# Kernel optimization log

Measured on AMD Instinct MI355X. Metric: run time of the kernel, lower is better.

## Reference

```python
import jax, jax.numpy as jnp
import numpy as np

B, N, IN_DIM, OUT_DIM, MID_DIM, K = 4, 8192, 3, 64, 32, 16
EPS = 1e-5  # BatchNorm eps


def _bn_relu(x, gamma, beta):
    # x: [B, N, C]; BatchNorm1d in training mode -> batch stats over (B, N)
    mean = jnp.mean(x, axis=(0, 1))
    var = jnp.var(x, axis=(0, 1))
    return jax.nn.relu(gamma * (x - mean) * jax.lax.rsqrt(var + EPS) + beta)


def _gather(pts, idx):
    # pts: [B, N, C]; idx: [B, ...] int -> [B, ..., C]
    return jax.vmap(lambda p, i: p[i])(pts, idx)


def _fps(xyz, npoint):
    # farthest point sampling; xyz: [B, N, 3] -> idx [B, npoint]
    b, n, _ = xyz.shape

    def step(carry, _):
        dist, farthest = carry
        centroid = jnp.take_along_axis(xyz, farthest[:, None, None], axis=1)  # [B,1,3]
        d = jnp.sum((xyz - centroid) ** 2, axis=-1)  # [B,N]
        dist = jnp.minimum(dist, d)
        nxt = jnp.argmax(dist, axis=-1).astype(jnp.int32)
        return (dist, nxt), farthest

    init = (jnp.full((b, n), 1e10, xyz.dtype), jnp.zeros((b,), jnp.int32))
    _, idx = jax.lax.scan(step, init, None, length=npoint)
    return idx.T  # [B, npoint]


def _knn(query, ref, k):
    # query: [B,S,3], ref: [B,N,3] -> k nearest indices [B,S,k]
    d = (jnp.sum(query ** 2, -1, keepdims=True)
         - 2.0 * jnp.einsum('bsd,bnd->bsn', query, ref)
         + jnp.sum(ref ** 2, -1)[:, None, :])
    _, idx = jax.lax.top_k(-d, k)
    return idx


def setup_inputs() -> dict:
    key = jax.random.key(0)
    ks = jax.random.split(key, 13)
    sc = lambda fan_in: 1.0 / np.sqrt(fan_in)
    inp = {
        'x_in': jax.random.normal(ks[0], (B, N, IN_DIM), jnp.float32),
        # first_mlp: Conv1d(3,32,1) -> BN -> ReLU -> Conv1d(32,64,1)
        'W1': jax.random.uniform(ks[1], (MID_DIM, IN_DIM), jnp.float32, -sc(IN_DIM), sc(IN_DIM)),
        'b1': jax.random.uniform(ks[2], (MID_DIM,), jnp.float32, -sc(IN_DIM), sc(IN_DIM)),
        'g1': jnp.ones((MID_DIM,), jnp.float32),
        'be1': jnp.zeros((MID_DIM,), jnp.float32),
        'W2': jax.random.uniform(ks[3], (OUT_DIM, MID_DIM), jnp.float32, -sc(MID_DIM), sc(MID_DIM)),
        'b2': jax.random.uniform(ks[4], (OUT_DIM,), jnp.float32, -sc(MID_DIM), sc(MID_DIM)),
        # last_mlp: Conv1d(67,64,1) -> BN -> ReLU -> Conv1d(64,64,1)
        'W3': jax.random.uniform(ks[5], (OUT_DIM, OUT_DIM + IN_DIM), jnp.float32, -sc(OUT_DIM + IN_DIM), sc(OUT_DIM + IN_DIM)),
        'b3': jax.random.uniform(ks[6], (OUT_DIM,), jnp.float32, -sc(OUT_DIM + IN_DIM), sc(OUT_DIM + IN_DIM)),
        'g2': jnp.ones((OUT_DIM,), jnp.float32),
        'be2': jnp.zeros((OUT_DIM,), jnp.float32),
        'W4': jax.random.uniform(ks[7], (OUT_DIM, OUT_DIM), jnp.float32, -sc(OUT_DIM), sc(OUT_DIM)),
        'b4': jax.random.uniform(ks[8], (OUT_DIM,), jnp.float32, -sc(OUT_DIM), sc(OUT_DIM)),
    }
    return inp


def reference(x_in, W1, b1, g1, be1, W2, b2, W3, b3, g2, be2, W4, b4):
    # first_mlp (1x1 convs == per-point matmuls), [B,N,3] -> [B,N,64]
    h = _bn_relu(x_in @ W1.T + b1, g1, be1)
    feat = h @ W2.T + b2  # [B,N,64]

    # sample_and_group: FPS to N//2 centers, kNN grouping (indices are non-diff)
    xyz_c = jax.lax.stop_gradient(x_in)
    npoint = N // 2
    fidx = _fps(xyz_c, npoint)                      # [B,S]
    new_xyz = _gather(x_in, fidx)                   # [B,S,3]
    idx = _knn(_gather(xyz_c, fidx), xyz_c, K)      # [B,S,K]

    grouped_xyz = _gather(x_in, idx) - new_xyz[:, :, None, :]  # [B,S,K,3]
    grouped_feat = _gather(feat, idx)                          # [B,S,K,64]
    x_cat = jnp.concatenate([grouped_xyz, grouped_feat], axis=-1)  # [B,S,K,67]

    x = jnp.max(x_cat, axis=2)  # max over neighbors -> [B,S,67]

    # last_mlp, [B,S,67] -> [B,S,64]
    x = _bn_relu(x @ W3.T + b3, g2, be2)
    return x @ W4.T + b4
```

## Files before the change

### kernel.cpp

```cpp
#include <hip/hip_runtime.h>
#include <float.h>
#include <math.h>

#define NB 4
#define NPTS 8192
#define NS 4096
#define MIDC 32
#define OUTC 64
#define CATC 67
#define BN_EPS 1e-5f
#define TOTAL_PTS (NB*NPTS)
#define TOTAL_S (NB*NS)
#define KT2 1024
#define N_FEATX_ITEMS 128
#define N_KNN_ITEMS 256
#define N_WORKERS 128

__device__ __forceinline__ double packkey(double d, int sp) {
    return __longlong_as_double((__double_as_longlong(d) & 0xFFFFFFFFFFFFE000ULL)
                                | (unsigned long long)sp);
}

template<int CTRL, int RM>
__device__ __forceinline__ double dpp_fmax64(double v) {
    int lo = __builtin_amdgcn_update_dpp(0, __double2loint(v), CTRL, RM, 0xF, false);
    int hi = __builtin_amdgcn_update_dpp(0, __double2hiint(v), CTRL, RM, 0xF, false);
    return fmax(v, __hiloint2double(hi, lo));
}

__device__ __forceinline__ unsigned int mpart(unsigned int x) {
    x &= 1023u;
    x = (x | (x << 16)) & 0x030000FFu;
    x = (x | (x << 8))  & 0x0300F00Fu;
    x = (x | (x << 4))  & 0x030C30C3u;
    x = (x | (x << 2))  & 0x09249249u;
    return x;
}

__global__ void k_init(float* __restrict__ stats, double* __restrict__ mom, int* __restrict__ ctrs) {
    int tid = threadIdx.x;
    if (tid < 128) stats[64 + tid] = 0.f;
    if (tid < 9) mom[tid] = 0.0;
    if (tid < 2) ctrs[tid] = 0;
}

__global__ void __launch_bounds__(256) k_mom(const float* __restrict__ xin, double* __restrict__ mom) {
    int t = blockIdx.x * 256 + threadIdx.x;
    double sx = 0, sy = 0, sz = 0, sxx = 0, sxy = 0, sxz = 0, syy = 0, syz = 0, szz = 0;
#pragma unroll
    for (int j = 0; j < 4; j++) {
        int p = t * 4 + j;
        double x = (double)xin[p * 3], y = (double)xin[p * 3 + 1], z = (double)xin[p * 3 + 2];
        sx += x; sy += y; sz += z;
        sxx = fma(x, x, sxx); sxy = fma(x, y, sxy); sxz = fma(x, z, sxz);
        syy = fma(y, y, syy); syz = fma(y, z, syz); szz = fma(z, z, szz);
    }
#pragma unroll
    for (int off = 32; off; off >>= 1) {
        sx += __shfl_down(sx, off); sy += __shfl_down(sy, off); sz += __shfl_down(sz, off);
        sxx += __shfl_down(sxx, off); sxy += __shfl_down(sxy, off); sxz += __shfl_down(sxz, off);
        syy += __shfl_down(syy, off); syz += __shfl_down(syz, off); szz += __shfl_down(szz, off);
    }
    if ((threadIdx.x & 63) == 0) {
        atomicAdd(&mom[0], sx); atomicAdd(&mom[1], sy); atomicAdd(&mom[2], sz);
        atomicAdd(&mom[3], sxx); atomicAdd(&mom[4], sxy); atomicAdd(&mom[5], sxz);
        atomicAdd(&mom[6], syy); atomicAdd(&mom[7], syz); atomicAdd(&mom[8], szz);
    }
}

__global__ void k_bn1stats(const double* __restrict__ mom, const float* __restrict__ W1,
                           const float* __restrict__ b1, float* __restrict__ stats) {
    int c = threadIdx.x;
    double n = (double)TOTAL_PTS;
    double mx = mom[0] / n, my = mom[1] / n, mz = mom[2] / n;
    double Cxx = mom[3] / n - mx * mx, Cxy = mom[4] / n - mx * my, Cxz = mom[5] / n - mx * mz;
    double Cyy = mom[6] / n - my * my, Cyz = mom[7] / n - my * mz, Czz = mom[8] / n - mz * mz;
    double wx = (double)W1[c * 3], wy = (double)W1[c * 3 + 1], wz = (double)W1[c * 3 + 2];
    double mu = wx * mx + wy * my + wz * mz + (double)b1[c];
    double var = wx * wx * Cxx + wy * wy * Cyy + wz * wz * Czz
               + 2.0 * (wx * wy * Cxy + wx * wz * Cxz + wy * wz * Cyz);
    stats[c] = (float)mu;
    stats[32 + c] = rsqrtf(fmaxf((float)var, 0.f) + BN_EPS);
}

union MU {
    struct { float4 spts[NPTS]; double swd[2][16]; float bbx[16][6]; } f;
    struct { float sxf[KT2], syf[KT2], szf[KT2]; double mk[4][16][64]; } k;
    struct { float W2s[OUTC * MIDC]; float w1s[MIDC * 3], b1s[MIDC], p1[MIDC], p2[MIDC]; } x;
    struct { float W3s[OUTC * CATC]; float x67[4][68]; float lsum[64], lsq[64]; } g;
};

__device__ void do_fps(MU& u, const float* __restrict__ xin, int* __restrict__ fidx) {
    const int b = blockIdx.x;
    const int tid = threadIdx.x;
    const int lane = tid & 63, w = tid >> 6;
    const float* xb = xin + (size_t)b * NPTS * 3;

    float mnx = FLT_MAX, mny = FLT_MAX, mnz = FLT_MAX;
    float mxx = -FLT_MAX, mxy = -FLT_MAX, mxz = -FLT_MAX;
    for (int j = 0; j < 8; j++) {
        int p = tid + (j << 10);
        float x = xb[p * 3], y = xb[p * 3 + 1], z = xb[p * 3 + 2];
        mnx = fminf(mnx, x); mny = fminf(mny, y); mnz = fminf(mnz, z);
        mxx = fmaxf(mxx, x); mxy = fmaxf(mxy, y); mxz = fmaxf(mxz, z);
    }
#pragma unroll
    for (int off = 32; off; off >>= 1) {
        mnx = fminf(mnx, __shfl_xor(mnx, off)); mny = fminf(mny, __shfl_xor(mny, off));
        mnz = fminf(mnz, __shfl_xor(mnz, off));
        mxx = fmaxf(mxx, __shfl_xor(mxx, off)); mxy = fmaxf(mxy, __shfl_xor(mxy, off));
        mxz = fmaxf(mxz, __shfl_xor(mxz, off));
    }
    if (lane == 0) {
        u.f.bbx[w][0] = mnx; u.f.bbx[w][1] = mny; u.f.bbx[w][2] = mnz;
        u.f.bbx[w][3] = mxx; u.f.bbx[w][4] = mxy; u.f.bbx[w][5] = mxz;
    }
    __syncthreads();
#pragma unroll
    for (int i = 0; i < 16; i++) {
        mnx = fminf(mnx, u.f.bbx[i][0]); mny = fminf(mny, u.f.bbx[i][1]);
        mnz = fminf(mnz, u.f.bbx[i][2]);
        mxx = fmaxf(mxx, u.f.bbx[i][3]); mxy = fmaxf(mxy, u.f.bbx[i][4]);
        mxz = fmaxf(mxz, u.f.bbx[i][5]);
    }
    float scx = 1023.0f / fmaxf(mxx - mnx, 1e-20f);
    float scy = 1023.0f / fmaxf(mxy - mny, 1e-20f);
    float scz = 1023.0f / fmaxf(mxz - mnz, 1e-20f);
    __syncthreads();

    unsigned long long* karr = (unsigned long long*)&u;
    for (int j = 0; j < 8; j++) {
        int p = tid + (j << 10);
        float x = xb[p * 3], y = xb[p * 3 + 1], z = xb[p * 3 + 2];
        unsigned int ix = (unsigned int)min(1023, max(0, (int)((x - mnx) * scx)));
        unsigned int iy = (unsigned int)min(1023, max(0, (int)((y - mny) * scy)));
        unsigned int iz = (unsigned int)min(1023, max(0, (int)((z - mnz) * scz)));
        unsigned long long code = (unsigned long long)((mpart(ix) << 2) | (mpart(iy) << 1) | mpart(iz));
        karr[p] = (code << 13) | (unsigned long long)p;
    }
    __syncthreads();
    for (int k = 2; k <= NPTS; k <<= 1) {
        for (int jj = k >> 1; jj > 0; jj >>= 1) {
            for (int pos = tid; pos < NPTS; pos += 1024) {
                int l2 = pos ^ jj;
                if (l2 > pos) {
                    unsigned long long a = karr[pos], c = karr[l2];
                    bool up = ((pos & k) == 0);
                    if ((up && a > c) || (!up && a < c)) { karr[pos] = c; karr[l2] = a; }
                }
            }
            __syncthreads();
        }
    }

    unsigned long long kk[8];
#pragma unroll
    for (int j = 0; j < 8; j++) kk[j] = karr[tid * 8 + j];
    __syncthreads();
    float blox = FLT_MAX, bloy = FLT_MAX, bloz = FLT_MAX;
    float bhix = -FLT_MAX, bhiy = -FLT_MAX, bhiz = -FLT_MAX;
    double dk[8];
#pragma unroll
    for (int j = 0; j < 8; j++) {
        int oi = (int)(kk[j] & 0x1FFFULL);
        float x = xb[oi * 3], y = xb[oi * 3 + 1], z = xb[oi * 3 + 2];
        int sp = tid * 8 + j;
        int slot = (sp >> 3) | ((sp & 7) << 10);
        u.f.spts[slot] = make_float4(x, y, z, __int_as_float(oi));
        blox = fminf(blox, x); bloy = fminf(bloy, y); bloz = fminf(bloz, z);
        bhix = fmaxf(bhix, x); bhiy = fmaxf(bhiy, y); bhiz = fmaxf(bhiz, z);
        dk[j] = packkey(1e10, sp);
    }
    if (tid == 0)
        __hip_atomic_store(&fidx[b * NS], 0, __ATOMIC_RELAXED, __HIP_MEMORY_SCOPE_AGENT);
    __syncthreads();

    float cxf = xb[0], cyf = xb[1], czf = xb[2];
    double cx = (double)cxf, cy = (double)cyf, cz = (double)czf;
    double tmax = packkey(1e10, tid * 8 + 7);
    double wm = 0.0;
    for (int t = 1; t < NS; t++) {
        float exf = fmaxf(fmaxf(blox - cxf, cxf - bhix), 0.f);
        float eyf = fmaxf(fmaxf(bloy - cyf, cyf - bhiy), 0.f);
        float ezf = fmaxf(fmaxf(bloz - czf, czf - bhiz), 0.f);
        float dmsqf = fmaf(exf, exf, fmaf(eyf, eyf, ezf * ezf));
        double tupper = __longlong_as_double(__double_as_longlong(tmax) | 0x1FFFULL);
        bool doupd = !((double)dmsqf * 0.99999 > tupper);
        if (__any(doupd)) {
            if (doupd) {
                double t0 = 0.0, t1 = 0.0;
#pragma unroll
                for (int j = 0; j < 8; j += 2) {
                    float4 v0 = u.f.spts[tid | (j << 10)];
                    float4 v1 = u.f.spts[tid | ((j + 1) << 10)];
                    double dx0 = (double)v0.x - cx, dy0 = (double)v0.y - cy, dz0 = (double)v0.z - cz;
                    double d0 = fma(dx0, dx0, fma(dy0, dy0, dz0 * dz0));
                    double nk0 = fmin(dk[j], packkey(d0, tid * 8 + j));
                    dk[j] = nk0; t0 = fmax(t0, nk0);
                    double dx1 = (double)v1.x - cx, dy1 = (double)v1.y - cy, dz1 = (double)v1.z - cz;
                    double d1 = fma(dx1, dx1, fma(dy1, dy1, dz1 * dz1));
                    double nk1 = fmin(dk[j + 1], packkey(d1, tid * 8 + j + 1));
                    dk[j + 1] = nk1; t1 = fmax(t1, nk1);
                }
                tmax = fmax(t0, t1);
            }
            double v = tmax;
            v = dpp_fmax64<0x121, 0xF>(v);
            v = dpp_fmax64<0x122, 0xF>(v);
            v = dpp_fmax64<0x124, 0xF>(v);
            v = dpp_fmax64<0x128, 0xF>(v);
            v = dpp_fmax64<0x142, 0xa>(v);
            v = dpp_fmax64<0x143, 0x8>(v);
            int wlo = __builtin_amdgcn_readlane(__double2loint(v), 63);
            int whi = __builtin_amdgcn_readlane(__double2hiint(v), 63);
            wm = __hiloint2double(whi, wlo);
        }
        if (lane == 0) u.f.swd[t & 1][w] = wm;
        __syncthreads();
        double gv = u.f.swd[t & 1][lane & 15];
        gv = dpp_fmax64<0x121, 0xF>(gv);
        gv = dpp_fmax64<0x122, 0xF>(gv);
        gv = dpp_fmax64<0x124, 0xF>(gv);
        gv = dpp_fmax64<0x128, 0xF>(gv);
        int sp = (int)((unsigned int)__double_as_longlong(gv) & 0x1FFFu);
        float4 cw = u.f.spts[(sp >> 3) | ((sp & 7) << 10)];
        cxf = cw.x; cyf = cw.y; czf = cw.z;
        cx = (double)cxf; cy = (double)cyf; cz = (double)czf;
        if (tid == 0)
            __hip_atomic_store(&fidx[b * NS + t], __float_as_int(cw.w),
                               __ATOMIC_RELAXED, __HIP_MEMORY_SCOPE_AGENT);
    }
}

__device__ void do_featx(MU& u, int item, const float* __restrict__ xin, const float* __restrict__ stats,
                         const float* __restrict__ W1, const float* __restrict__ b1,
                         const float* __restrict__ g1, const float* __restrict__ be1,
                         const float* __restrict__ W2, const float* __restrict__ b2,
                         float* __restrict__ feat, int* __restrict__ ctrs) {
    int tid = threadIdx.x;
    for (int i = tid; i < OUTC * MIDC; i += 256) u.x.W2s[i] = W2[i];
    if (tid < MIDC * 3) u.x.w1s[tid] = W1[tid];
    if (tid < MIDC) {
        u.x.b1s[tid] = b1[tid];
        u.x.p1[tid] = stats[32 + tid] * g1[tid];
        u.x.p2[tid] = be1[tid] - stats[tid] * stats[32 + tid] * g1[tid];
    }
    __syncthreads();
    int p = item * 256 + tid;
    float x = xin[p * 3], y = xin[p * 3 + 1], z = xin[p * 3 + 2];
    float h[MIDC];
#pragma unroll
    for (int c = 0; c < MIDC; c++) {
        float v = fmaf(u.x.w1s[c * 3 + 2], z, fmaf(u.x.w1s[c * 3 + 1], y, fmaf(u.x.w1s[c * 3], x, u.x.b1s[c])));
        h[c] = fmaxf(fmaf(v, u.x.p1[c], u.x.p2[c]), 0.f);
    }
#pragma unroll 4
    for (int o = 0; o < OUTC; o++) {
        float a = b2[o];
#pragma unroll
        for (int c = 0; c < MIDC; c++) a = fmaf(u.x.W2s[o * MIDC + c], h[c], a);
        feat[p * OUTC + o] = a;
    }
    __syncthreads();
    if (tid == 0)
        __hip_atomic_fetch_add(&ctrs[1], 1, __ATOMIC_RELEASE, __HIP_MEMORY_SCOPE_AGENT);
}

__device__ void do_knn_group(MU& u, int* qarr, int item, const float* __restrict__ xin,
                             const int* __restrict__ fidx, int* __restrict__ knn,
                             const float* __restrict__ feat,
                             const float* __restrict__ W3, const float* __restrict__ b3,
                             float* __restrict__ y3, float* __restrict__ stats,
                             int* __restrict__ ctrs) {
    int tid = threadIdx.x;
    int part = tid >> 6;
    int ql = tid & 63;
    int b = (item * 64) >> 12;
    const float* xb = xin + (size_t)b * NPTS * 3;
    if (tid < 64) {
        unsigned int qv;
        for (;;) {
            qv = (unsigned int)__hip_atomic_load(&fidx[item * 64 + tid],
                                                 __ATOMIC_RELAXED, __HIP_MEMORY_SCOPE_AGENT);
            if (qv <= 8191u) break;
            __builtin_amdgcn_s_sleep(64);
        }
        qarr[tid] = (int)qv;
    }
    __syncthreads();
    int qi = qarr[ql];
    float qxf = xb[qi * 3], qyf = xb[qi * 3 + 1], qzf = xb[qi * 3 + 2];
    double qx = (double)qxf, qy = (double)qyf, qz = (double)qzf;
    double kd0 = DBL_MAX, kd1 = DBL_MAX, kd2 = DBL_MAX, kd3 = DBL_MAX,
           kd4 = DBL_MAX, kd5 = DBL_MAX, kd6 = DBL_MAX, kd7 = DBL_MAX,
           kd8 = DBL_MAX, kd9 = DBL_MAX, kd10 = DBL_MAX, kd11 = DBL_MAX,
           kd12 = DBL_MAX, kd13 = DBL_MAX, kd14 = DBL_MAX, kd15 = DBL_MAX;
    float kd15f = FLT_MAX;
    for (int tile = 0; tile < NPTS / KT2; tile++) {
        for (int m = tid; m < KT2; m += 256) {
            int gj = tile * KT2 + m;
            u.k.sxf[m] = xb[gj * 3]; u.k.syf[m] = xb[gj * 3 + 1]; u.k.szf[m] = xb[gj * 3 + 2];
        }
        __syncthreads();
        int base = part * (KT2 / 4);
        for (int m = 0; m < KT2 / 4; m++) {
            int li = base + m;
            float fdx = qxf - u.k.sxf[li], fdy = qyf - u.k.syf[li], fdz = qzf - u.k.szf[li];
            float d32 = fmaf(fdx, fdx, fmaf(fdy, fdy, fdz * fdz));
            if (d32 <= kd15f) {
                double dx = qx - (double)u.k.sxf[li], dy = qy - (double)u.k.syf[li], dz = qz - (double)u.k.szf[li];
                double d = fma(dx, dx, fma(dy, dy, dz * dz));
                double key = __longlong_as_double(
                    (__double_as_longlong(d) & 0xFFFFFFFFFFFFE000ULL)
                    | (unsigned long long)(tile * KT2 + li));
                if (key < kd15) {
                    kd15 = fmax(kd14, fmin(kd15, key)); kd14 = fmax(kd13, fmin(kd14, key));
                    kd13 = fmax(kd12, fmin(kd13, key)); kd12 = fmax(kd11, fmin(kd12, key));
                    kd11 = fmax(kd10, fmin(kd11, key)); kd10 = fmax(kd9,  fmin(kd10, key));
                    kd9  = fmax(kd8,  fmin(kd9,  key)); kd8  = fmax(kd7,  fmin(kd8,  key));
                    kd7  = fmax(kd6,  fmin(kd7,  key)); kd6  = fmax(kd5,  fmin(kd6,  key));
                    kd5  = fmax(kd4,  fmin(kd5,  key)); kd4  = fmax(kd3,  fmin(kd4,  key));
                    kd3  = fmax(kd2,  fmin(kd3,  key)); kd2  = fmax(kd1,  fmin(kd2,  key));
                    kd1  = fmax(kd0,  fmin(kd1,  key)); kd0  = fmin(kd0,  key);
                    kd15f = (kd15 >= DBL_MAX) ? FLT_MAX
                          : __double2float_ru(kd15) * (1.0f + 1e-5f);
                }
            }
        }
        __syncthreads();
    }
    u.k.mk[part][0][ql] = kd0;  u.k.mk[part][1][ql] = kd1;  u.k.mk[part][2][ql] = kd2;  u.k.mk[part][3][ql] = kd3;
    u.k.mk[part][4][ql] = kd4;  u.k.mk[part][5][ql] = kd5;  u.k.mk[part][6][ql] = kd6;  u.k.mk[part][7][ql] = kd7;
    u.k.mk[part][8][ql] = kd8;  u.k.mk[part][9][ql] = kd9;  u.k.mk[part][10][ql] = kd10; u.k.mk[part][11][ql] = kd11;
    u.k.mk[part][12][ql] = kd12; u.k.mk[part][13][ql] = kd13; u.k.mk[part][14][ql] = kd14; u.k.mk[part][15][ql] = kd15;
    __syncthreads();
    if (tid < 64) {
        int i0 = 0, i1 = 0, i2 = 0, i3 = 0;
        double h0 = u.k.mk[0][0][tid], h1 = u.k.mk[1][0][tid], h2 = u.k.mk[2][0][tid], h3 = u.k.mk[3][0][tid];
        int* outp = knn + (size_t)(item * 64 + tid) * 16;
#pragma unroll
        for (int k = 0; k < 16; k++) {
            double mm = fmin(fmin(h0, h1), fmin(h2, h3));
            outp[k] = (int)(__double_as_longlong(mm) & 0x1FFFULL);
            if (mm == h0)      { i0++; h0 = (i0 < 16) ? u.k.mk[0][i0][tid] : DBL_MAX; }
            else if (mm == h1) { i1++; h1 = (i1 < 16) ? u.k.mk[1][i1][tid] : DBL_MAX; }
            else if (mm == h2) { i2++; h2 = (i2 < 16) ? u.k.mk[2][i2][tid] : DBL_MAX; }
            else               { i3++; h3 = (i3 < 16) ? u.k.mk[3][i3][tid] : DBL_MAX; }
        }
    }
    if (tid == 0) {
        while (__hip_atomic_load(&ctrs[1], __ATOMIC_ACQUIRE, __HIP_MEMORY_SCOPE_AGENT) < N_FEATX_ITEMS)
            __builtin_amdgcn_s_sleep(64);
    }
    __syncthreads();

    int w = tid >> 6, lane = tid & 63;
    for (int i = tid; i < OUTC * CATC; i += 256) u.g.W3s[i] = W3[i];
    if (tid < 64) { u.g.lsum[tid] = 0.f; u.g.lsq[tid] = 0.f; }
    __syncthreads();
    float bb3 = b3[lane];
    float psum = 0.f, psq = 0.f;
    int p0 = item * 64 + w * 16;
    for (int it = 0; it < 16; it++) {
        int p = p0 + it;
        int pb = p >> 12;
        int myidx = knn[p * 16 + (lane & 15)];
        int nbk[16];
#pragma unroll
        for (int k = 0; k < 16; k++) nbk[k] = __shfl(myidx, k);
        float m = -FLT_MAX;
#pragma unroll
        for (int k = 0; k < 16; k++) m = fmaxf(m, feat[(size_t)(pb * NPTS + nbk[k]) * OUTC + lane]);
        u.g.x67[w][3 + lane] = m;
        if (lane < 3) {
            int ci = qarr[w * 16 + it];
            float cc = xin[(size_t)(pb * NPTS + ci) * 3 + lane];
            float mg = -FLT_MAX;
#pragma unroll
            for (int k = 0; k < 16; k++) mg = fmaxf(mg, xin[(size_t)(pb * NPTS + nbk[k]) * 3 + lane] - cc);
            u.g.x67[w][lane] = mg;
        }
        float acc = bb3;
#pragma unroll
        for (int c = 0; c < CATC; c++) acc = fmaf(u.g.W3s[lane * CATC + c], u.g.x67[w][c], acc);
        y3[(size_t)p * OUTC + lane] = acc;
        psum += acc; psq = fmaf(acc, acc, psq);
    }
    atomicAdd(&u.g.lsum[lane], psum);
    atomicAdd(&u.g.lsq[lane], psq);
    __syncthreads();
    if (tid < 64) { atomicAdd(&stats[64 + tid], u.g.lsum[tid]); atomicAdd(&stats[128 + tid], u.g.lsq[tid]); }
}

__global__ void __launch_bounds__(1024) k_mega(const float* __restrict__ xin,
                                               const float* __restrict__ W1, const float* __restrict__ b1,
                                               const float* __restrict__ g1, const float* __restrict__ be1,
                                               const float* __restrict__ W2, const float* __restrict__ b2,
                                               const float* __restrict__ W3, const float* __restrict__ b3,
                                               float* __restrict__ stats, float* __restrict__ feat,
                                               int* __restrict__ fidx, int* __restrict__ knn,
                                               float* __restrict__ y3, int* __restrict__ ctrs) {
    __shared__ MU u;
    __shared__ int s_item;
    __shared__ int qarr[64];
    if (blockIdx.x < NB) { do_fps(u, xin, fidx); return; }
    if (threadIdx.x >= 256) return;
    int tid = threadIdx.x;
    for (;;) {
        __syncthreads();
        if (tid == 0) s_item = atomicAdd(&ctrs[0], 1);
        __syncthreads();
        int item = s_item;
        if (item >= N_FEATX_ITEMS + N_KNN_ITEMS) return;
        if (item < N_FEATX_ITEMS)
            do_featx(u, item, xin, stats, W1, b1, g1, be1, W2, b2, feat, ctrs);
        else
            do_knn_group(u, qarr, item - N_FEATX_ITEMS, xin, fidx, knn, feat, W3, b3, y3, stats, ctrs);
    }
}

__global__ void k_stats2(float* __restrict__ stats) {
    int c = threadIdx.x;
    float m = stats[64 + c] / (float)TOTAL_S;
    float var = stats[128 + c] / (float)TOTAL_S - m * m;
    stats[192 + c] = m;
    stats[256 + c] = rsqrtf(var + BN_EPS);
}

__global__ void __launch_bounds__(256) k_last(const float* __restrict__ y3, const float* __restrict__ stats,
                                              const float* __restrict__ g2, const float* __restrict__ be2,
                                              const float* __restrict__ W4, const float* __restrict__ b4,
                                              float* __restrict__ out) {
    __shared__ float W4t[OUTC * OUTC];
    __shared__ float xs[4][64];
    int tid = threadIdx.x;
    for (int i = tid; i < OUTC * OUTC; i += 256) W4t[(i & 63) * 64 + (i >> 6)] = W4[i];
    int lp = tid >> 6, o = tid & 63;
    int p = blockIdx.x * 4 + lp;
    float v = y3[(size_t)p * OUTC + o];
    v = fmaf((v - stats[192 + o]) * stats[256 + o], g2[o], be2[o]);
    xs[lp][o] = fmaxf(v, 0.f);
    __syncthreads();
    const float* xp = xs[lp];
    float acc = b4[o];
#pragma unroll
    for (int c = 0; c < OUTC; c++) acc = fmaf(W4t[c * 64 + o], xp[c], acc);
    out[(size_t)p * OUTC + o] = acc;
}

extern "C" void kernel_launch(void* const* d_in, const int* in_sizes, int n_in,
                              void* d_out, int out_size, void* d_ws, size_t ws_size,
                              hipStream_t stream) {
    const float* xin = (const float*)d_in[0];
    const float* W1  = (const float*)d_in[1];
    const float* b1  = (const float*)d_in[2];
    const float* g1  = (const float*)d_in[3];
    const float* be1 = (const float*)d_in[4];
    const float* W2  = (const float*)d_in[5];
    const float* b2  = (const float*)d_in[6];
    const float* W3  = (const float*)d_in[7];
    const float* b3  = (const float*)d_in[8];
    const float* g2  = (const float*)d_in[9];
    const float* be2 = (const float*)d_in[10];
    const float* W4  = (const float*)d_in[11];
    const float* b4  = (const float*)d_in[12];
    float* out = (float*)d_out;

    float* ws = (float*)d_ws;
    float* feat = ws;
    int*   fidx = (int*)(feat + (size_t)TOTAL_PTS * OUTC);
    int*   knn  = fidx + TOTAL_S;
    float* y3   = (float*)(knn + (size_t)TOTAL_S * 16);
    float* stats = y3 + (size_t)TOTAL_S * OUTC;
    double* mom = (double*)(stats + 320);
    int* ctrs = (int*)(mom + 9);

    k_init<<<1, 256, 0, stream>>>(stats, mom, ctrs);
    k_mom<<<32, 256, 0, stream>>>(xin, mom);
    k_bn1stats<<<1, 32, 0, stream>>>(mom, W1, b1, stats);
    k_mega<<<NB + N_WORKERS, 1024, 0, stream>>>(xin, W1, b1, g1, be1, W2, b2, W3, b3,
                                                stats, feat, fidx, knn, y3, ctrs);
    k_stats2<<<1, 64, 0, stream>>>(stats);
    k_last<<<TOTAL_S / 4, 256, 0, stream>>>(y3, stats, g2, be2, W4, b4, out);
}
```

Baseline: 4.283 ms.

## Fold moment, BN stats, and final MLP stages into persistent mega-kernel work queue

Moves the moment reduction, BN1 stats, BN2 stats and final MLP into the persistent k_mega work queue as ordered item ranges, gated by global atomic counters with acquire/release spin-waits. This removes four separate kernel launches and the gaps between them. Worker block count is cut from 128 to 32, which reduces parallelism for the featx/knn/last items that run alongside FPS. Spin-waiting blocks may sit idle while dependencies finish.

```diff
diff --git a/kernel.cpp b/kernel.cpp
--- a/kernel.cpp
+++ b/kernel.cpp
@@ -12,9 +12,17 @@
 #define TOTAL_PTS (NB*NPTS)
 #define TOTAL_S (NB*NS)
 #define KT2 1024
+#define N_WORKERS 32
+
+#define IT_MOM0   0
+#define IT_BN1    32
+#define IT_FEATX0 33
+#define IT_KNN0   161
+#define IT_STATS2 417
+#define IT_LAST0  418
+#define IT_END    674
 #define N_FEATX_ITEMS 128
 #define N_KNN_ITEMS 256
-#define N_WORKERS 128
 
 __device__ __forceinline__ double packkey(double d, int sp) {
     return __longlong_as_double((__double_as_longlong(d) & 0xFFFFFFFFFFFFE000ULL)
@@ -41,46 +49,7 @@
     int tid = threadIdx.x;
     if (tid < 128) stats[64 + tid] = 0.f;
     if (tid < 9) mom[tid] = 0.0;
-    if (tid < 2) ctrs[tid] = 0;
-}
-
-__global__ void __launch_bounds__(256) k_mom(const float* __restrict__ xin, double* __restrict__ mom) {
-    int t = blockIdx.x * 256 + threadIdx.x;
-    double sx = 0, sy = 0, sz = 0, sxx = 0, sxy = 0, sxz = 0, syy = 0, syz = 0, szz = 0;
-#pragma unroll
-    for (int j = 0; j < 4; j++) {
-        int p = t * 4 + j;
-        double x = (double)xin[p * 3], y = (double)xin[p * 3 + 1], z = (double)xin[p * 3 + 2];
-        sx += x; sy += y; sz += z;
-        sxx = fma(x, x, sxx); sxy = fma(x, y, sxy); sxz = fma(x, z, sxz);
-        syy = fma(y, y, syy); syz = fma(y, z, syz); szz = fma(z, z, szz);
-    }
-#pragma unroll
-    for (int off = 32; off; off >>= 1) {
-        sx += __shfl_down(sx, off); sy += __shfl_down(sy, off); sz += __shfl_down(sz, off);
-        sxx += __shfl_down(sxx, off); sxy += __shfl_down(sxy, off); sxz += __shfl_down(sxz, off);
-        syy += __shfl_down(syy, off); syz += __shfl_down(syz, off); szz += __shfl_down(szz, off);
-    }
-    if ((threadIdx.x & 63) == 0) {
-        atomicAdd(&mom[0], sx); atomicAdd(&mom[1], sy); atomicAdd(&mom[2], sz);
-        atomicAdd(&mom[3], sxx); atomicAdd(&mom[4], sxy); atomicAdd(&mom[5], sxz);
-        atomicAdd(&mom[6], syy); atomicAdd(&mom[7], syz); atomicAdd(&mom[8], szz);
-    }
-}
-
-__global__ void k_bn1stats(const double* __restrict__ mom, const float* __restrict__ W1,
-                           const float* __restrict__ b1, float* __restrict__ stats) {
-    int c = threadIdx.x;
-    double n = (double)TOTAL_PTS;
-    double mx = mom[0] / n, my = mom[1] / n, mz = mom[2] / n;
-    double Cxx = mom[3] / n - mx * mx, Cxy = mom[4] / n - mx * my, Cxz = mom[5] / n - mx * mz;
-    double Cyy = mom[6] / n - my * my, Cyz = mom[7] / n - my * mz, Czz = mom[8] / n - mz * mz;
-    double wx = (double)W1[c * 3], wy = (double)W1[c * 3 + 1], wz = (double)W1[c * 3 + 2];
-    double mu = wx * mx + wy * my + wz * mz + (double)b1[c];
-    double var = wx * wx * Cxx + wy * wy * Cyy + wz * wz * Czz
-               + 2.0 * (wx * wy * Cxy + wx * wz * Cxz + wy * wz * Cyz);
-    stats[c] = (float)mu;
-    stats[32 + c] = rsqrtf(fmaxf((float)var, 0.f) + BN_EPS);
+    if (tid < 6) ctrs[tid] = 0;
 }
 
 union MU {
@@ -88,6 +57,7 @@
     struct { float sxf[KT2], syf[KT2], szf[KT2]; double mk[4][16][64]; } k;
     struct { float W2s[OUTC * MIDC]; float w1s[MIDC * 3], b1s[MIDC], p1[MIDC], p2[MIDC]; } x;
     struct { float W3s[OUTC * CATC]; float x67[4][68]; float lsum[64], lsq[64]; } g;
+    struct { float W4t[OUTC * OUTC]; float xs[4][64]; } l;
 };
 
 __device__ void do_fps(MU& u, const float* __restrict__ xin, int* __restrict__ fidx) {
@@ -232,12 +202,73 @@
     }
 }
 
+__device__ void do_mom(int item, const float* __restrict__ xin, double* __restrict__ mom,
+                       int* __restrict__ ctrs) {
+    int tid = threadIdx.x;
+    int t = item * 256 + tid;
+    double sx = 0, sy = 0, sz = 0, sxx = 0, sxy = 0, sxz = 0, syy = 0, syz = 0, szz = 0;
+#pragma unroll
+    for (int j = 0; j < 4; j++) {
+        int p = t * 4 + j;
+        double x = (double)xin[p * 3], y = (double)xin[p * 3 + 1], z = (double)xin[p * 3 + 2];
+        sx += x; sy += y; sz += z;
+        sxx = fma(x, x, sxx); sxy = fma(x, y, sxy); sxz = fma(x, z, sxz);
+        syy = fma(y, y, syy); syz = fma(y, z, syz); szz = fma(z, z, szz);
+    }
+#pragma unroll
+    for (int off = 32; off; off >>= 1) {
+        sx += __shfl_down(sx, off); sy += __shfl_down(sy, off); sz += __shfl_down(sz, off);
+        sxx += __shfl_down(sxx, off); sxy += __shfl_down(sxy, off); sxz += __shfl_down(sxz, off);
+        syy += __shfl_down(syy, off); syz += __shfl_down(syz, off); szz += __shfl_down(szz, off);
+    }
+    if ((tid & 63) == 0) {
+        atomicAdd(&mom[0], sx); atomicAdd(&mom[1], sy); atomicAdd(&mom[2], sz);
+        atomicAdd(&mom[3], sxx); atomicAdd(&mom[4], sxy); atomicAdd(&mom[5], sxz);
+        atomicAdd(&mom[6], syy); atomicAdd(&mom[7], syz); atomicAdd(&mom[8], szz);
+    }
+    __syncthreads();
+    if (tid == 0)
+        __hip_atomic_fetch_add(&ctrs[4], 1, __ATOMIC_RELEASE, __HIP_MEMORY_SCOPE_AGENT);
+}
+
+__device__ void do_bn1(const double* __restrict__ mom, const float* __restrict__ W1,
+                       const float* __restrict__ b1, float* __restrict__ stats,
+                       int* __restrict__ ctrs) {
+    int tid = threadIdx.x;
+    if (tid == 0) {
+        while (__hip_atomic_load(&ctrs[4], __ATOMIC_ACQUIRE, __HIP_MEMORY_SCOPE_AGENT) < 32)
+            __builtin_amdgcn_s_sleep(32);
+    }
+    __syncthreads();
+    if (tid < MIDC) {
+        int c = tid;
+        double n = (double)TOTAL_PTS;
+        double mx = mom[0] / n, my = mom[1] / n, mz = mom[2] / n;
+        double Cxx = mom[3] / n - mx * mx, Cxy = mom[4] / n - mx * my, Cxz = mom[5] / n - mx * mz;
+        double Cyy = mom[6] / n - my * my, Cyz = mom[7] / n - my * mz, Czz = mom[8] / n - mz * mz;
+        double wx = (double)W1[c * 3], wy = (double)W1[c * 3 + 1], wz = (double)W1[c * 3 + 2];
+        double mu = wx * mx + wy * my + wz * mz + (double)b1[c];
+        double var = wx * wx * Cxx + wy * wy * Cyy + wz * wz * Czz
+                   + 2.0 * (wx * wy * Cxy + wx * wz * Cxz + wy * wz * Cyz);
+        stats[c] = (float)mu;
+        stats[32 + c] = rsqrtf(fmaxf((float)var, 0.f) + BN_EPS);
+    }
+    __syncthreads();
+    if (tid == 0)
+        __hip_atomic_store(&ctrs[5], 1, __ATOMIC_RELEASE, __HIP_MEMORY_SCOPE_AGENT);
+}
+
 __device__ void do_featx(MU& u, int item, const float* __restrict__ xin, const float* __restrict__ stats,
                          const float* __restrict__ W1, const float* __restrict__ b1,
                          const float* __restrict__ g1, const float* __restrict__ be1,
                          const float* __restrict__ W2, const float* __restrict__ b2,
                          float* __restrict__ feat, int* __restrict__ ctrs) {
     int tid = threadIdx.x;
+    if (tid == 0) {
+        while (__hip_atomic_load(&ctrs[5], __ATOMIC_ACQUIRE, __HIP_MEMORY_SCOPE_AGENT) < 1)
+            __builtin_amdgcn_s_sleep(32);
+    }
+    __syncthreads();
     for (int i = tid; i < OUTC * MIDC; i += 256) u.x.W2s[i] = W2[i];
     if (tid < MIDC * 3) u.x.w1s[tid] = W1[tid];
     if (tid < MIDC) {
@@ -390,6 +421,55 @@
     atomicAdd(&u.g.lsq[lane], psq);
     __syncthreads();
     if (tid < 64) { atomicAdd(&stats[64 + tid], u.g.lsum[tid]); atomicAdd(&stats[128 + tid], u.g.lsq[tid]); }
+    __syncthreads();
+    if (tid == 0)
+        __hip_atomic_fetch_add(&ctrs[2], 1, __ATOMIC_RELEASE, __HIP_MEMORY_SCOPE_AGENT);
+}
+
+__device__ void do_stats2(float* __restrict__ stats, int* __restrict__ ctrs) {
+    int tid = threadIdx.x;
+    if (tid == 0) {
+        while (__hip_atomic_load(&ctrs[2], __ATOMIC_ACQUIRE, __HIP_MEMORY_SCOPE_AGENT) < N_KNN_ITEMS)
+            __builtin_amdgcn_s_sleep(64);
+    }
+    __syncthreads();
+    if (tid < 64) {
+        int c = tid;
+        float m = stats[64 + c] / (float)TOTAL_S;
+        float var = stats[128 + c] / (float)TOTAL_S - m * m;
+        stats[192 + c] = m;
+        stats[256 + c] = rsqrtf(var + BN_EPS);
+    }
+    __syncthreads();
+    if (tid == 0)
+        __hip_atomic_store(&ctrs[3], 1, __ATOMIC_RELEASE, __HIP_MEMORY_SCOPE_AGENT);
+}
+
+__device__ void do_last(MU& u, int item, const float* __restrict__ y3, const float* __restrict__ stats,
+                        const float* __restrict__ g2, const float* __restrict__ be2,
+                        const float* __restrict__ W4, const float* __restrict__ b4,
+                        float* __restrict__ out, int* __restrict__ ctrs) {
+    int tid = threadIdx.x;
+    if (tid == 0) {
+        while (__hip_atomic_load(&ctrs[3], __ATOMIC_ACQUIRE, __HIP_MEMORY_SCOPE_AGENT) < 1)
+            __builtin_amdgcn_s_sleep(32);
+    }
+    __syncthreads();
+    for (int i = tid; i < OUTC * OUTC; i += 256) u.l.W4t[(i & 63) * 64 + (i >> 6)] = W4[i];
+    __syncthreads();
+    int lp = tid >> 6, o = tid & 63;
+    float s192 = stats[192 + o], s256 = stats[256 + o];
+    float gg = g2[o], bb = be2[o], b4o = b4[o];
+    for (int it = 0; it < 16; it++) {
+        int p = item * 64 + it * 4 + lp;
+        float v = y3[(size_t)p * OUTC + o];
+        v = fmaf((v - s192) * s256, gg, bb);
+        u.l.xs[lp][o] = fmaxf(v, 0.f);
+        float acc = b4o;
+#pragma unroll
+        for (int c = 0; c < OUTC; c++) acc = fmaf(u.l.W4t[c * 64 + o], u.l.xs[lp][c], acc);
+        out[(size_t)p * OUTC + o] = acc;
+    }
 }
 
 __global__ void __launch_bounds__(1024) k_mega(const float* __restrict__ xin,
@@ -397,9 +477,12 @@
                                                const float* __restrict__ g1, const float* __restrict__ be1,
                                                const float* __restrict__ W2, const float* __restrict__ b2,
                                                const float* __restrict__ W3, const float* __restrict__ b3,
+                                               const float* __restrict__ g2, const float* __restrict__ be2,
+                                               const float* __restrict__ W4, const float* __restrict__ b4,
                                                float* __restrict__ stats, float* __restrict__ feat,
                                                int* __restrict__ fidx, int* __restrict__ knn,
-                                               float* __restrict__ y3, int* __restrict__ ctrs) {
+                                               float* __restrict__ y3, double* __restrict__ mom,
+                                               int* __restrict__ ctrs, float* __restrict__ out) {
     __shared__ MU u;
     __shared__ int s_item;
     __shared__ int qarr[64];
@@ -411,41 +494,20 @@
         if (tid == 0) s_item = atomicAdd(&ctrs[0], 1);
         __syncthreads();
         int item = s_item;
-        if (item >= N_FEATX_ITEMS + N_KNN_ITEMS) return;
-        if (item < N_FEATX_ITEMS)
-            do_featx(u, item, xin, stats, W1, b1, g1, be1, W2, b2, feat, ctrs);
+        if (item >= IT_END) return;
+        if (item < IT_BN1)
+            do_mom(item, xin, mom, ctrs);
+        else if (item == IT_BN1)
+            do_bn1(mom, W1, b1, stats, ctrs);
+        else if (item < IT_KNN0)
+            do_featx(u, item - IT_FEATX0, xin, stats, W1, b1, g1, be1, W2, b2, feat, ctrs);
+        else if (item < IT_STATS2)
+            do_knn_group(u, qarr, item - IT_KNN0, xin, fidx, knn, feat, W3, b3, y3, stats, ctrs);
+        else if (item == IT_STATS2)
+            do_stats2(stats, ctrs);
         else
-            do_knn_group(u, qarr, item - N_FEATX_ITEMS, xin, fidx, knn, feat, W3, b3, y3, stats, ctrs);
-    }
-}
-
-__global__ void k_stats2(float* __restrict__ stats) {
-    int c = threadIdx.x;
-    float m = stats[64 + c] / (float)TOTAL_S;
-    float var = stats[128 + c] / (float)TOTAL_S - m * m;
-    stats[192 + c] = m;
-    stats[256 + c] = rsqrtf(var + BN_EPS);
-}
-
-__global__ void __launch_bounds__(256) k_last(const float* __restrict__ y3, const float* __restrict__ stats,
-                                              const float* __restrict__ g2, const float* __restrict__ be2,
-                                              const float* __restrict__ W4, const float* __restrict__ b4,
-                                              float* __restrict__ out) {
-    __shared__ float W4t[OUTC * OUTC];
-    __shared__ float xs[4][64];
-    int tid = threadIdx.x;
-    for (int i = tid; i < OUTC * OUTC; i += 256) W4t[(i & 63) * 64 + (i >> 6)] = W4[i];
-    int lp = tid >> 6, o = tid & 63;
-    int p = blockIdx.x * 4 + lp;
-    float v = y3[(size_t)p * OUTC + o];
-    v = fmaf((v - stats[192 + o]) * stats[256 + o], g2[o], be2[o]);
-    xs[lp][o] = fmaxf(v, 0.f);
-    __syncthreads();
-    const float* xp = xs[lp];
-    float acc = b4[o];
-#pragma unroll
-    for (int c = 0; c < OUTC; c++) acc = fmaf(W4t[c * 64 + o], xp[c], acc);
-    out[(size_t)p * OUTC + o] = acc;
+            do_last(u, item - IT_LAST0, y3, stats, g2, be2, W4, b4, out, ctrs);
+    }
 }
 
 extern "C" void kernel_launch(void* const* d_in, const int* in_sizes, int n_in,
@@ -476,10 +538,7 @@
     int* ctrs = (int*)(mom + 9);
 
     k_init<<<1, 256, 0, stream>>>(stats, mom, ctrs);
-    k_mom<<<32, 256, 0, stream>>>(xin, mom);
-    k_bn1stats<<<1, 32, 0, stream>>>(mom, W1, b1, stats);
     k_mega<<<NB + N_WORKERS, 1024, 0, stream>>>(xin, W1, b1, g1, be1, W2, b2, W3, b3,
-                                                stats, feat, fidx, knn, y3, ctrs);
-    k_stats2<<<1, 64, 0, stream>>>(stats);
-    k_last<<<TOTAL_S / 4, 256, 0, stream>>>(y3, stats, g2, be2, W4, b4, out);
-}
+                                                g2, be2, W4, b4,
+                                                stats, feat, fidx, knn, y3, mom, ctrs, out);
+}
```

After: 6.996 ms. +63.3%, slower.
